# Kernel optimization log

Hardware: AMD Instinct MI355X
Metric: run time of the kernel (lower is better)

## Reference

```python
import jax, jax.numpy as jnp
import numpy as np

N = 100000   # num 'note' nodes
E = 1000000  # edges per relation
R = 3        # relation types (onset, consecutive, during)
IN = 128
OUT = 64
NEG_SLOPE = 0.2  # GATConv default leaky_relu slope


def setup_inputs() -> dict:
    key = jax.random.key(0)
    ks = jax.random.split(key, 13)
    x = jax.random.normal(ks[0], (N, IN), jnp.float32)
    ei0 = jax.random.randint(ks[1], (2, E), 0, N)
    ei1 = jax.random.randint(ks[2], (2, E), 0, N)
    ei2 = jax.random.randint(ks[3], (2, E), 0, N)
    s1 = 1.0 / np.sqrt(IN)
    s2 = 1.0 / np.sqrt(OUT)
    W1 = jax.random.normal(ks[4], (R, IN, OUT), jnp.float32) * s1
    a_src1 = jax.random.normal(ks[5], (R, OUT), jnp.float32) * s2
    a_dst1 = jax.random.normal(ks[6], (R, OUT), jnp.float32) * s2
    b1 = jnp.zeros((R, OUT), jnp.float32)
    W2 = jax.random.normal(ks[7], (R, OUT, OUT), jnp.float32) * s2
    a_src2 = jax.random.normal(ks[8], (R, OUT), jnp.float32) * s2
    a_dst2 = jax.random.normal(ks[9], (R, OUT), jnp.float32) * s2
    b2 = jnp.zeros((R, OUT), jnp.float32)
    return dict(x=x, ei0=ei0, ei1=ei1, ei2=ei2,
                W1=W1, a_src1=a_src1, a_dst1=a_dst1, b1=b1,
                W2=W2, a_src2=a_src2, a_dst2=a_dst2, b2=b2)


def _gat_relation(x, ei, W, a_src, a_dst, b):
    # single-head GATConv for one relation (aggr='sum' over edges)
    h = x @ W                              # [N, OUT]
    src, dst = ei[0], ei[1]
    al_src = h @ a_src                     # [N]
    al_dst = h @ a_dst                     # [N]
    e = jax.nn.leaky_relu(al_src[src] + al_dst[dst], NEG_SLOPE)  # [E]
    # segment softmax over incoming edges per destination node
    m = jax.ops.segment_max(e, dst, num_segments=N)              # [N]
    num = jnp.exp(e - m[dst])                                    # [E]
    den = jax.ops.segment_sum(num, dst, num_segments=N)          # [N]
    coef = num / den[dst]                                        # [E]
    msg = coef[:, None] * h[src]                                 # [E, OUT]
    return jax.ops.segment_sum(msg, dst, num_segments=N) + b     # [N, OUT]


def _hetero_layer(x, eis, W, a_src, a_dst, b):
    # to_hetero: per-relation GATConv, then mean across relations
    outs = [_gat_relation(x, eis[r], W[r], a_src[r], a_dst[r], b[r]) for r in range(R)]
    return jnp.mean(jnp.stack(outs, 0), 0)


def _l2norm(v):
    # F.normalize(v, dim=-1), eps=1e-12
    n = jnp.linalg.norm(v, axis=-1, keepdims=True)
    return v / jnp.maximum(n, 1e-12)


def reference(x, ei0, ei1, ei2, W1, a_src1, a_dst1, b1, W2, a_src2, a_dst2, b2):
    eis = [ei0, ei1, ei2]
    h = _hetero_layer(x, eis, W1, a_src1, a_dst1, b1)
    h = jax.nn.relu(_l2norm(h))  # dropout is identity in eval mode
    out = _hetero_layer(h, eis, W2, a_src2, a_dst2, b2)
    return out  # x_dict['note']
```

## Files before the change

### kernel.cpp

```cpp
#include <hip/hip_runtime.h>
#include <hip/hip_bf16.h>
#include <hip/hip_fp16.h>
#include <math.h>

constexpr int NN = 100000;
constexpr int EE = 1000000;
constexpr int RRR = 3;
constexpr int DIN = 128;
constexpr int DOUT = 64;
constexpr float SLOPE = 0.2f;
constexpr int NR = RRR * NN;
constexpr int BSEG = 256;
constexpr int NBUCK = (NR + BSEG - 1) / BSEG;
constexpr int BCAP = 4096;
constexpr int CHUNK_E = 4096;
constexpr int NCH_PER_R = (EE + CHUNK_E - 1) / CHUNK_E;
constexpr int NCH = RRR * NCH_PER_R;
constexpr int MT = NBUCK * NCH;
constexpr int SCAN_CHUNK = 1024;
constexpr int NSCB = (MT + SCAN_CHUNK - 1) / SCAN_CHUNK;
constexpr int GEMM_BLKS = (NN + 63) / 64;

using f16x8 = __attribute__((ext_vector_type(8))) _Float16;
using f32x4 = __attribute__((ext_vector_type(4))) float;

template<int CTRL>
__device__ __forceinline__ float dppf(float v) {
    return __int_as_float(__builtin_amdgcn_update_dpp(
        __float_as_int(v), __float_as_int(v), CTRL, 0xf, 0xf, false));
}
__device__ __forceinline__ float dpp_allred_add16(float v) {
    v += dppf<0xB1>(v);
    v += dppf<0x4E>(v);
    v += dppf<0x141>(v);
    v += dppf<0x140>(v);
    return v;
}

__global__ __launch_bounds__(256) void pack_W(
    const float* __restrict__ W1, const float* __restrict__ W2,
    const float* __restrict__ b1, const float* __restrict__ b2,
    __half* __restrict__ Wp1, __half* __restrict__ Wp2,
    float* __restrict__ bs1, float* __restrict__ bs2)
{
    int r = blockIdx.x;
    for (int i = threadIdx.x; i < 4 * 4 * 512; i += 256) {
        int j = i & 7, lane = (i >> 3) & 63, nt = (i >> 9) & 3, ks = i >> 11;
        int k = ks * 32 + (lane >> 4) * 8 + j, c = nt * 16 + (lane & 15);
        Wp1[((size_t)r * 16 + ks * 4 + nt) * 512 + lane * 8 + j] = __float2half(W1[(r * DIN + k) * 64 + c]);
    }
    for (int i = threadIdx.x; i < 2 * 4 * 512; i += 256) {
        int j = i & 7, lane = (i >> 3) & 63, nt = (i >> 9) & 3, ks = i >> 11;
        int k = ks * 32 + (lane >> 4) * 8 + j, c = nt * 16 + (lane & 15);
        Wp2[((size_t)r * 8 + ks * 4 + nt) * 512 + lane * 8 + j] = __float2half(W2[(r * DOUT + k) * 64 + c]);
    }
    if (r == 0) {
        for (int c = threadIdx.x; c < 64; c += 256) {
            bs1[c] = (b1[c] + b1[64 + c] + b1[128 + c]) * (1.f / 3.f);
            bs2[c] = (b2[c] + b2[64 + c] + b2[128 + c]) * (1.f / 3.f);
        }
    }
}

template<int K, typename AT>
__device__ __forceinline__ void gemm_body(
    int gbid,
    const AT* __restrict__ xin,
    const __half* __restrict__ Wp,
    const float* __restrict__ asrc, const float* __restrict__ adst,
    __half* __restrict__ h,
    float* __restrict__ als, float* __restrict__ ald)
{
    constexpr int KS = K / 32;
    __shared__ float outb[64 * 65];
    const int t = threadIdx.x;
    const int lane = t & 63;
    const int w = t >> 6;
    const int row0 = gbid * 64;

    const int kgrp = lane >> 4;
    const int l15 = lane & 15;
    int arow = row0 + w * 16 + l15; if (arow >= NN) arow = NN - 1;

    f16x8 a[KS];
    if constexpr (sizeof(AT) == 2) {
        const __half* ab = (const __half*)xin + (size_t)arow * K + kgrp * 8;
#pragma unroll
        for (int ks = 0; ks < KS; ++ks) a[ks] = *(const f16x8*)(ab + ks * 32);
    } else {
        const float* ab = (const float*)xin + (size_t)arow * K + kgrp * 8;
#pragma unroll
        for (int ks = 0; ks < KS; ++ks) {
            float4 lo = *(const float4*)(ab + ks * 32);
            float4 hi = *(const float4*)(ab + ks * 32 + 4);
            union { f16x8 v; __half2 p[4]; } u;
            u.p[0] = __floats2half2_rn(lo.x, lo.y);
            u.p[1] = __floats2half2_rn(lo.z, lo.w);
            u.p[2] = __floats2half2_rn(hi.x, hi.y);
            u.p[3] = __floats2half2_rn(hi.z, hi.w);
            a[ks] = u.v;
        }
    }

    const int nrows = (NN - row0 < 64) ? (NN - row0) : 64;

#pragma unroll
    for (int r = 0; r < RRR; ++r) {
        const __half* wbase = Wp + ((size_t)r * KS * 4) * 512 + lane * 8;
        f32x4 acc[4] = {};
#pragma unroll
        for (int ks = 0; ks < KS; ++ks) {
#pragma unroll
            for (int nt = 0; nt < 4; ++nt) {
                f16x8 b = *(const f16x8*)(wbase + (size_t)(ks * 4 + nt) * 512);
                acc[nt] = __builtin_amdgcn_mfma_f32_16x16x32_f16(a[ks], b, acc[nt], 0, 0, 0);
            }
        }

        {
            float ps[4] = {0.f, 0.f, 0.f, 0.f}, pd[4] = {0.f, 0.f, 0.f, 0.f};
#pragma unroll
            for (int nt = 0; nt < 4; ++nt) {
                int c = l15 + 16 * nt;
                float a_ = asrc[r * 64 + c], d_ = adst[r * 64 + c];
#pragma unroll
                for (int i = 0; i < 4; ++i) {
                    ps[i] = fmaf(acc[nt][i], a_, ps[i]);
                    pd[i] = fmaf(acc[nt][i], d_, pd[i]);
                }
            }
#pragma unroll
            for (int o = 8; o; o >>= 1) {
#pragma unroll
                for (int i = 0; i < 4; ++i) {
                    ps[i] += __shfl_xor(ps[i], o);
                    pd[i] += __shfl_xor(pd[i], o);
                }
            }
            if (l15 == 0) {
#pragma unroll
                for (int i = 0; i < 4; ++i) {
                    int row = row0 + w * 16 + kgrp * 4 + i;
                    if (row < NN) { als[r * NN + row] = ps[i]; ald[r * NN + row] = pd[i]; }
                }
            }
        }

#pragma unroll
        for (int nt = 0; nt < 4; ++nt)
#pragma unroll
            for (int i = 0; i < 4; ++i)
                outb[(w * 16 + kgrp * 4 + i) * 65 + l15 + 16 * nt] = acc[nt][i];
        __syncthreads();

        __half2* h2 = (__half2*)(h + ((size_t)r * NN + row0) * 64);
        for (int idx = t; idx < nrows * 32; idx += 256) {
            int row = idx >> 5, cc = idx & 31;
            h2[row * 32 + cc] = __floats2half2_rn(outb[row * 65 + cc * 2], outb[row * 65 + cc * 2 + 1]);
        }
        __syncthreads();
    }
}

__device__ __forceinline__ void hist_body(
    int hb,
    const int* __restrict__ ei0, const int* __restrict__ ei1, const int* __restrict__ ei2,
    unsigned* __restrict__ M)
{
    __shared__ unsigned hist[NBUCK];
    const int r = hb / NCH_PER_R, bx = hb % NCH_PER_R;
    const int* ei = (r == 0) ? ei0 : ((r == 1) ? ei1 : ei2);
    const int t = threadIdx.x;
    for (int i = t; i < NBUCK; i += 256) hist[i] = 0;
    __syncthreads();
    const int e0 = bx * CHUNK_E;
    const int e1 = (e0 + CHUNK_E < EE) ? e0 + CHUNK_E : EE;
    for (int e = e0 + t; e < e1; e += 256) {
        int idx = r * NN + ei[EE + e];
        atomicAdd(&hist[idx >> 8], 1u);
    }
    __syncthreads();
    const int c = r * NCH_PER_R + bx;
    for (int i = t; i < NBUCK; i += 256) M[(size_t)i * NCH + c] = hist[i];
}

__global__ __launch_bounds__(256) void fused_prep(
    const float* __restrict__ x, const __half* __restrict__ Wp1,
    const float* __restrict__ as1, const float* __restrict__ ad1,
    __half* __restrict__ h, float* __restrict__ als, float* __restrict__ ald,
    const int* __restrict__ ei0, const int* __restrict__ ei1, const int* __restrict__ ei2,
    unsigned* __restrict__ M)
{
    if ((int)blockIdx.x < GEMM_BLKS)
        gemm_body<DIN, float>(blockIdx.x, x, Wp1, as1, ad1, h, als, ald);
    else
        hist_body(blockIdx.x - GEMM_BLKS, ei0, ei1, ei2, M);
}

template<int K, typename AT>
__global__ __launch_bounds__(256) void gemm_mfma2(
    const AT* __restrict__ xin, const __half* __restrict__ Wp,
    const float* __restrict__ asrc, const float* __restrict__ adst,
    __half* __restrict__ h, float* __restrict__ als, float* __restrict__ ald)
{
    gemm_body<K, AT>(blockIdx.x, xin, Wp, asrc, adst, h, als, ald);
}

__global__ __launch_bounds__(256) void scan_block(unsigned* __restrict__ data, unsigned* __restrict__ bsum)
{
    __shared__ unsigned tsum[256];
    const int base = blockIdx.x * SCAN_CHUNK;
    const int t = threadIdx.x;
    const int i0 = base + t * 4;
    unsigned v[4];
#pragma unroll
    for (int k = 0; k < 4; ++k) v[k] = (i0 + k < MT) ? data[i0 + k] : 0u;
    unsigned run = 0;
#pragma unroll
    for (int k = 0; k < 4; ++k) { unsigned x = v[k]; v[k] = run; run += x; }
    tsum[t] = run;
    __syncthreads();
    unsigned val = run;
    for (int d = 1; d < 256; d <<= 1) {
        unsigned add = (t >= d) ? tsum[t - d] : 0u;
        __syncthreads();
        val += add;
        tsum[t] = val;
        __syncthreads();
    }
    unsigned texcl = val - run;
    if (t == 255) bsum[blockIdx.x] = val;
#pragma unroll
    for (int k = 0; k < 4; ++k)
        if (i0 + k < MT) data[i0 + k] = texcl + v[k];
}

__global__ __launch_bounds__(256) void scan_add(unsigned* __restrict__ data, const unsigned* __restrict__ bsum)
{
    __shared__ unsigned red[256];
    const int b = blockIdx.x, t = threadIdx.x;
    unsigned part = 0;
    for (int j = t; j < b; j += 256) part += bsum[j];
    red[t] = part;
    __syncthreads();
    for (int s = 128; s; s >>= 1) {
        if (t < s) red[t] += red[t + s];
        __syncthreads();
    }
    unsigned P = red[0];
    const int i0 = b * SCAN_CHUNK + t * 4;
#pragma unroll
    for (int k = 0; k < 4; ++k)
        if (i0 + k < MT) data[i0 + k] += P;
}

__global__ __launch_bounds__(256) void chunk_scatter(
    const int* __restrict__ ei0, const int* __restrict__ ei1, const int* __restrict__ ei2,
    const unsigned* __restrict__ Ms, unsigned* __restrict__ packed)
{
    __shared__ unsigned cur[NBUCK];
    const int r = blockIdx.y, bx = blockIdx.x;
    const int* ei = (r == 0) ? ei0 : ((r == 1) ? ei1 : ei2);
    const int t = threadIdx.x;
    const int c = r * NCH_PER_R + bx;
    for (int i = t; i < NBUCK; i += 256) cur[i] = Ms[(size_t)i * NCH + c];
    __syncthreads();
    const int e0 = bx * CHUNK_E;
    const int e1 = (e0 + CHUNK_E < EE) ? e0 + CHUNK_E : EE;
    for (int e = e0 + t; e < e1; e += 256) {
        int src = ei[e];
        int idx = r * NN + ei[EE + e];
        unsigned pos = atomicAdd(&cur[idx >> 8], 1u);
        packed[pos] = (unsigned)src | ((unsigned)(idx & 255) << 24);
    }
}

__global__ __launch_bounds__(256) void bucket_build(
    unsigned* __restrict__ packed,
    const unsigned* __restrict__ Ms,
    unsigned* __restrict__ off)
{
    __shared__ unsigned sp[BCAP];
    __shared__ unsigned ssrc[BCAP];
    __shared__ unsigned scnt[BSEG];
    __shared__ unsigned scur[BSEG];
    __shared__ unsigned tsum[BSEG];
    const int b = blockIdx.x;
    const int t = threadIdx.x;
    const unsigned base = Ms[(size_t)b * NCH];
    const unsigned next = (b + 1 < NBUCK) ? Ms[(size_t)(b + 1) * NCH] : (unsigned)((size_t)RRR * EE);
    int cnt = (int)(next - base);
    if (cnt > BCAP) cnt = BCAP;
    for (int i = t; i < cnt; i += 256) sp[i] = packed[base + i];
    scnt[t] = 0;
    __syncthreads();
    for (int i = t; i < cnt; i += 256) atomicAdd(&scnt[sp[i] >> 24], 1u);
    __syncthreads();
    unsigned v = scnt[t];
    tsum[t] = v;
    __syncthreads();
    unsigned val = v;
    for (int d = 1; d < 256; d <<= 1) {
        unsigned add = (t >= d) ? tsum[t - d] : 0u;
        __syncthreads();
        val += add;
        tsum[t] = val;
        __syncthreads();
    }
    unsigned excl = val - v;
    scur[t] = excl;
    const int segs = (NR - b * BSEG < BSEG) ? (NR - b * BSEG) : BSEG;
    if (t < segs) off[b * BSEG + t] = base + excl;
    __syncthreads();
    for (int i = t; i < cnt; i += 256) {
        unsigned p = sp[i];
        unsigned pos = atomicAdd(&scur[p >> 24], 1u);
        ssrc[pos] = p & 0x00FFFFFFu;
    }
    __syncthreads();
    for (int i = t; i < cnt; i += 256) packed[base + i] = ssrc[i];
}

template<bool L1>
__global__ __launch_bounds__(256) void aggregate10(
    const int* __restrict__ csr_src, const unsigned* __restrict__ off,
    const __half* __restrict__ h,
    const float* __restrict__ als, const float* __restrict__ ald,
    const float* __restrict__ bsum3,
    float* __restrict__ outp,
    __half* __restrict__ outH)
{
    __shared__ float sbuf[4][64];
    const int wid = threadIdx.x >> 6;
    const int lane = threadIdx.x & 63;
    const int nh = lane >> 5;
    const int l31 = lane & 31;
    const int sub = l31 >> 4;
    const int fc = l31 & 15;
    const int node = blockIdx.x * 8 + wid * 2 + nh;

    unsigned start[RRR]; int cnt[RRR]; float aldv[RRR];
    int maxcnt = 0;
#pragma unroll
    for (int r = 0; r < RRR; ++r) {
        int idx = r * NN + node;
        unsigned s = off[idx];
        unsigned e = (idx == NR - 1) ? (unsigned)((size_t)RRR * EE) : off[idx + 1];
        start[r] = s; cnt[r] = (int)(e - s); aldv[r] = ald[idx];
        if (cnt[r] > maxcnt) maxcnt = cnt[r];
    }

    float4 total = make_float4(0.f, 0.f, 0.f, 0.f);

    if (__all(maxcnt <= 32)) {
        int srcv[RRR]; float p[RRR], den[RRR];
#pragma unroll
        for (int r = 0; r < RRR; ++r) {
            bool act = l31 < cnt[r];
            int s_ = act ? csr_src[start[r] + l31] : 0;
            srcv[r] = s_;
            float sv = act ? (als[r * NN + s_] + aldv[r]) : -3.0e38f;
            float lr = (sv > 0.f) ? sv : SLOPE * sv;
            lr = fminf(lr, 60.f);
            p[r] = __expf(lr);
            den[r] = dpp_allred_add16(p[r]);
        }
#pragma unroll
        for (int r = 0; r < RRR; ++r) den[r] += __shfl_xor(den[r], 16);
#pragma unroll
        for (int r = 0; r < RRR; ++r) {
            float inv = (cnt[r] > 0) ? 1.f / den[r] : 0.f;
            p[r] *= inv;
        }

        float4 acc = make_float4(0.f, 0.f, 0.f, 0.f);
#pragma unroll
        for (int r = 0; r < RRR; ++r) {
            const __half* hr = h + (size_t)r * NN * DOUT;
            const int nq = (cnt[r] + 7) >> 3;
            for (int q = 0; q < nq; ++q) {
                const int base = q * 8;
                float pl[4]; int sl[4];
#pragma unroll
                for (int l = 0; l < 4; ++l) {
                    int e = base + l * 2 + sub;
                    pl[l] = __shfl(p[r], nh * 32 + e);
                    sl[l] = __shfl(srcv[r], nh * 32 + e);
                }
                uint2 rl[4];
#pragma unroll
                for (int l = 0; l < 4; ++l)
                    rl[l] = *(const uint2*)(hr + (size_t)sl[l] * DOUT + fc * 4);
#pragma unroll
                for (int l = 0; l < 4; ++l) {
                    float2 f01 = __half22float2(*(const __half2*)&rl[l].x);
                    float2 f23 = __half22float2(*(const __half2*)&rl[l].y);
                    acc.x = fmaf(pl[l], f01.x, acc.x);
                    acc.y = fmaf(pl[l], f01.y, acc.y);
                    acc.z = fmaf(pl[l], f23.x, acc.z);
                    acc.w = fmaf(pl[l], f23.y, acc.w);
                }
            }
        }
        acc.x += __shfl_xor(acc.x, 16); acc.y += __shfl_xor(acc.y, 16);
        acc.z += __shfl_xor(acc.z, 16); acc.w += __shfl_xor(acc.w, 16);
        total = acc;
    } else {
        for (int nn = 0; nn < 2; ++nn) {
            int node2 = blockIdx.x * 8 + wid * 2 + nn;
            float totalS = 0.f;
#pragma unroll
            for (int r = 0; r < RRR; ++r) {
                int idx = r * NN + node2;
                unsigned s2 = off[idx];
                unsigned e2 = (idx == NR - 1) ? (unsigned)((size_t)RRR * EE) : off[idx + 1];
                int c2 = (int)(e2 - s2);
                if (c2 <= 0) continue;
                float aldv2 = ald[idx];
                const __half* hr = h + (size_t)r * NN * DOUT;
                const float* alsr = als + (size_t)r * NN;
                float m = -3.4e38f, den = 0.f, accv = 0.f;
                for (int t0 = 0; t0 < c2; t0 += 64) {
                    int j = t0 + lane;
                    bool act = (j < c2);
                    int src = 0;
                    float lrv = -3.4e38f;
                    if (act) {
                        src = csr_src[s2 + j];
                        float sv = alsr[src] + aldv2;
                        lrv = (sv > 0.f) ? sv : SLOPE * sv;
                    }
                    float mt = lrv;
#pragma unroll
                    for (int o = 32; o; o >>= 1) mt = fmaxf(mt, __shfl_xor(mt, o));
                    float mnew = fmaxf(m, mt);
                    float scale = __expf(m - mnew);
                    den *= scale; accv *= scale; m = mnew;
                    float pp = act ? __expf(lrv - m) : 0.f;
                    float ps = pp;
#pragma unroll
                    for (int o = 32; o; o >>= 1) ps += __shfl_xor(ps, o);
                    den += ps;
                    int tcnt = c2 - t0; if (tcnt > 64) tcnt = 64;
                    for (int j2 = 0; j2 < tcnt; ++j2) {
                        int sj = __builtin_amdgcn_readlane(src, j2);
                        float pj = __int_as_float(__builtin_amdgcn_readlane(__float_as_int(pp), j2));
                        accv = fmaf(pj, __half2float(hr[(size_t)sj * DOUT + lane]), accv);
                    }
                }
                totalS += accv / den;
            }
            sbuf[wid][lane] = totalS;
            __builtin_amdgcn_s_waitcnt(0);
            if (nh == nn) total = *(const float4*)&sbuf[wid][fc * 4];
            __builtin_amdgcn_s_waitcnt(0);
        }
    }

    float4 bb = *(const float4*)(bsum3 + fc * 4);
    float4 v;
    v.x = fmaf(total.x, 1.f / 3.f, bb.x);
    v.y = fmaf(total.y, 1.f / 3.f, bb.y);
    v.z = fmaf(total.z, 1.f / 3.f, bb.z);
    v.w = fmaf(total.w, 1.f / 3.f, bb.w);
    if (L1) {
        float ss = v.x * v.x + v.y * v.y + v.z * v.z + v.w * v.w;
        ss = dpp_allred_add16(ss);
        float di = 1.f / fmaxf(sqrtf(ss), 1e-12f);
        v.x = fmaxf(v.x * di, 0.f);
        v.y = fmaxf(v.y * di, 0.f);
        v.z = fmaxf(v.z * di, 0.f);
        v.w = fmaxf(v.w * di, 0.f);
        if (sub == 0) {
            __half2* o2 = (__half2*)(outH + (size_t)node * DOUT + fc * 4);
            o2[0] = __floats2half2_rn(v.x, v.y);
            o2[1] = __floats2half2_rn(v.z, v.w);
        }
    } else {
        if (sub == 0) *(float4*)(outp + (size_t)node * DOUT + fc * 4) = v;
    }
}

extern "C" void kernel_launch(void* const* d_in, const int* in_sizes, int n_in,
                              void* d_out, int out_size, void* d_ws, size_t ws_size,
                              hipStream_t stream) {
    const float* x   = (const float*)d_in[0];
    const int* ei0   = (const int*)d_in[1];
    const int* ei1   = (const int*)d_in[2];
    const int* ei2   = (const int*)d_in[3];
    const float* W1  = (const float*)d_in[4];
    const float* as1 = (const float*)d_in[5];
    const float* ad1 = (const float*)d_in[6];
    const float* b1  = (const float*)d_in[7];
    const float* W2  = (const float*)d_in[8];
    const float* as2 = (const float*)d_in[9];
    const float* ad2 = (const float*)d_in[10];
    const float* b2  = (const float*)d_in[11];
    float* out = (float*)d_out;

    float* ws = (float*)d_ws;
    size_t off_u = 0;
    __half* h       = (__half*)(ws + off_u); off_u += (size_t)RRR * NN * DOUT / 2;
    float* als      = ws + off_u; off_u += (size_t)RRR * NN;
    float* ald      = ws + off_u; off_u += (size_t)RRR * NN;
    unsigned* packed= (unsigned*)(ws + off_u); off_u += (size_t)RRR * EE;
    unsigned* off   = (unsigned*)(ws + off_u); off_u += NR;
    __half* hmid_h  = (__half*)(ws + off_u); off_u += (size_t)NN * DOUT / 2;
    __half* Wp1     = (__half*)(ws + off_u); off_u += (3 * 16 * 512) / 2;
    __half* Wp2     = (__half*)(ws + off_u); off_u += (3 * 8 * 512) / 2;
    float* bs1      = ws + off_u; off_u += 64;
    float* bs2      = ws + off_u; off_u += 64;
    unsigned* M     = (unsigned*)(ws + off_u); off_u += MT;
    unsigned* bsum  = (unsigned*)(ws + off_u); off_u += NSCB + 8;

    dim3 blk(256);
    dim3 gC(NCH_PER_R, RRR);
    int gA = (NN + 7) / 8;

    pack_W<<<3, blk, 0, stream>>>(W1, W2, b1, b2, Wp1, Wp2, bs1, bs2);

    fused_prep<<<GEMM_BLKS + NCH, blk, 0, stream>>>(
        x, Wp1, as1, ad1, h, als, ald, ei0, ei1, ei2, M);

    scan_block<<<NSCB, blk, 0, stream>>>(M, bsum);
    scan_add<<<NSCB, blk, 0, stream>>>(M, bsum);
    chunk_scatter<<<gC, blk, 0, stream>>>(ei0, ei1, ei2, M, packed);
    bucket_build<<<NBUCK, blk, 0, stream>>>(packed, M, off);
    const int* csr_src = (const int*)packed;

    aggregate10<true><<<gA, blk, 0, stream>>>(csr_src, off, h, als, ald, bs1, out, hmid_h);

    gemm_mfma2<DOUT, __half><<<GEMM_BLKS, blk, 0, stream>>>(hmid_h, Wp2, as2, ad2, h, als, ald);
    aggregate10<false><<<gA, blk, 0, stream>>>(csr_src, off, h, als, ald, bs2, out, hmid_h);
}
```

Measured before the change: 256.8 us.

## Fuse CSR scan, scatter and bucket build into one cooperative kernel

Replaces four separate launches (block scan, scan add, chunk scatter, bucket build) with a single cooperative kernel that uses grid-wide syncs between phases, launched with NCH blocks. This removes per-kernel launch gaps and tail effects. In exchange, each grid.sync has its own cost, the scan and bucket phases now run with fewer blocks in grid-stride loops, and the 33KB shared allocation limits residency, which cooperative launch requires for all blocks.

```diff
diff --git a/kernel.cpp b/kernel.cpp
--- a/kernel.cpp
+++ b/kernel.cpp
@@ -1,7 +1,10 @@
 #include <hip/hip_runtime.h>
+#include <hip/hip_cooperative_groups.h>
 #include <hip/hip_bf16.h>
 #include <hip/hip_fp16.h>
 #include <math.h>
+
+namespace cg = cooperative_groups;
 
 constexpr int NN = 100000;
 constexpr int EE = 1000000;
@@ -206,119 +209,128 @@
     gemm_body<K, AT>(blockIdx.x, xin, Wp, asrc, adst, h, als, ald);
 }
 
-__global__ __launch_bounds__(256) void scan_block(unsigned* __restrict__ data, unsigned* __restrict__ bsum)
-{
-    __shared__ unsigned tsum[256];
-    const int base = blockIdx.x * SCAN_CHUNK;
+__global__ __launch_bounds__(256) void csr_finish(
+    const int* __restrict__ ei0, const int* __restrict__ ei1, const int* __restrict__ ei2,
+    unsigned* __restrict__ M, unsigned* __restrict__ bsum,
+    unsigned* __restrict__ packed, unsigned* __restrict__ off)
+{
+    __shared__ unsigned smem[2 * BCAP + 3 * BSEG];
+    cg::grid_group grid = cg::this_grid();
     const int t = threadIdx.x;
-    const int i0 = base + t * 4;
-    unsigned v[4];
-#pragma unroll
-    for (int k = 0; k < 4; ++k) v[k] = (i0 + k < MT) ? data[i0 + k] : 0u;
-    unsigned run = 0;
-#pragma unroll
-    for (int k = 0; k < 4; ++k) { unsigned x = v[k]; v[k] = run; run += x; }
-    tsum[t] = run;
-    __syncthreads();
-    unsigned val = run;
-    for (int d = 1; d < 256; d <<= 1) {
-        unsigned add = (t >= d) ? tsum[t - d] : 0u;
+    const int nb = gridDim.x;
+
+    {
+        unsigned* tsum = smem;
+        for (int b = blockIdx.x; b < NSCB; b += nb) {
+            __syncthreads();
+            const int i0 = b * SCAN_CHUNK + t * 4;
+            unsigned v[4];
+#pragma unroll
+            for (int k = 0; k < 4; ++k) v[k] = (i0 + k < MT) ? M[i0 + k] : 0u;
+            unsigned run = 0;
+#pragma unroll
+            for (int k = 0; k < 4; ++k) { unsigned x = v[k]; v[k] = run; run += x; }
+            tsum[t] = run;
+            __syncthreads();
+            unsigned val = run;
+            for (int d = 1; d < 256; d <<= 1) {
+                unsigned add = (t >= d) ? tsum[t - d] : 0u;
+                __syncthreads();
+                val += add;
+                tsum[t] = val;
+                __syncthreads();
+            }
+            unsigned texcl = val - run;
+            if (t == 255) bsum[b] = val;
+#pragma unroll
+            for (int k = 0; k < 4; ++k)
+                if (i0 + k < MT) M[i0 + k] = texcl + v[k];
+        }
+    }
+    grid.sync();
+
+    {
+        unsigned* red = smem;
+        for (int b = blockIdx.x; b < NSCB; b += nb) {
+            __syncthreads();
+            unsigned part = 0;
+            for (int j = t; j < b; j += 256) part += bsum[j];
+            red[t] = part;
+            __syncthreads();
+            for (int s = 128; s; s >>= 1) {
+                if (t < s) red[t] += red[t + s];
+                __syncthreads();
+            }
+            unsigned P = red[0];
+            const int i0 = b * SCAN_CHUNK + t * 4;
+#pragma unroll
+            for (int k = 0; k < 4; ++k)
+                if (i0 + k < MT) M[i0 + k] += P;
+        }
+    }
+    grid.sync();
+
+    {
+        unsigned* cur = smem;
+        const int hb = blockIdx.x;
+        const int r = hb / NCH_PER_R, bx = hb % NCH_PER_R;
+        const int* ei = (r == 0) ? ei0 : ((r == 1) ? ei1 : ei2);
         __syncthreads();
-        val += add;
-        tsum[t] = val;
+        for (int i = t; i < NBUCK; i += 256) cur[i] = M[(size_t)i * NCH + hb];
         __syncthreads();
-    }
-    unsigned texcl = val - run;
-    if (t == 255) bsum[blockIdx.x] = val;
-#pragma unroll
-    for (int k = 0; k < 4; ++k)
-        if (i0 + k < MT) data[i0 + k] = texcl + v[k];
-}
-
-__global__ __launch_bounds__(256) void scan_add(unsigned* __restrict__ data, const unsigned* __restrict__ bsum)
-{
-    __shared__ unsigned red[256];
-    const int b = blockIdx.x, t = threadIdx.x;
-    unsigned part = 0;
-    for (int j = t; j < b; j += 256) part += bsum[j];
-    red[t] = part;
-    __syncthreads();
-    for (int s = 128; s; s >>= 1) {
-        if (t < s) red[t] += red[t + s];
-        __syncthreads();
-    }
-    unsigned P = red[0];
-    const int i0 = b * SCAN_CHUNK + t * 4;
-#pragma unroll
-    for (int k = 0; k < 4; ++k)
-        if (i0 + k < MT) data[i0 + k] += P;
-}
-
-__global__ __launch_bounds__(256) void chunk_scatter(
-    const int* __restrict__ ei0, const int* __restrict__ ei1, const int* __restrict__ ei2,
-    const unsigned* __restrict__ Ms, unsigned* __restrict__ packed)
-{
-    __shared__ unsigned cur[NBUCK];
-    const int r = blockIdx.y, bx = blockIdx.x;
-    const int* ei = (r == 0) ? ei0 : ((r == 1) ? ei1 : ei2);
-    const int t = threadIdx.x;
-    const int c = r * NCH_PER_R + bx;
-    for (int i = t; i < NBUCK; i += 256) cur[i] = Ms[(size_t)i * NCH + c];
-    __syncthreads();
-    const int e0 = bx * CHUNK_E;
-    const int e1 = (e0 + CHUNK_E < EE) ? e0 + CHUNK_E : EE;
-    for (int e = e0 + t; e < e1; e += 256) {
-        int src = ei[e];
-        int idx = r * NN + ei[EE + e];
-        unsigned pos = atomicAdd(&cur[idx >> 8], 1u);
-        packed[pos] = (unsigned)src | ((unsigned)(idx & 255) << 24);
-    }
-}
-
-__global__ __launch_bounds__(256) void bucket_build(
-    unsigned* __restrict__ packed,
-    const unsigned* __restrict__ Ms,
-    unsigned* __restrict__ off)
-{
-    __shared__ unsigned sp[BCAP];
-    __shared__ unsigned ssrc[BCAP];
-    __shared__ unsigned scnt[BSEG];
-    __shared__ unsigned scur[BSEG];
-    __shared__ unsigned tsum[BSEG];
-    const int b = blockIdx.x;
-    const int t = threadIdx.x;
-    const unsigned base = Ms[(size_t)b * NCH];
-    const unsigned next = (b + 1 < NBUCK) ? Ms[(size_t)(b + 1) * NCH] : (unsigned)((size_t)RRR * EE);
-    int cnt = (int)(next - base);
-    if (cnt > BCAP) cnt = BCAP;
-    for (int i = t; i < cnt; i += 256) sp[i] = packed[base + i];
-    scnt[t] = 0;
-    __syncthreads();
-    for (int i = t; i < cnt; i += 256) atomicAdd(&scnt[sp[i] >> 24], 1u);
-    __syncthreads();
-    unsigned v = scnt[t];
-    tsum[t] = v;
-    __syncthreads();
-    unsigned val = v;
-    for (int d = 1; d < 256; d <<= 1) {
-        unsigned add = (t >= d) ? tsum[t - d] : 0u;
-        __syncthreads();
-        val += add;
-        tsum[t] = val;
-        __syncthreads();
-    }
-    unsigned excl = val - v;
-    scur[t] = excl;
-    const int segs = (NR - b * BSEG < BSEG) ? (NR - b * BSEG) : BSEG;
-    if (t < segs) off[b * BSEG + t] = base + excl;
-    __syncthreads();
-    for (int i = t; i < cnt; i += 256) {
-        unsigned p = sp[i];
-        unsigned pos = atomicAdd(&scur[p >> 24], 1u);
-        ssrc[pos] = p & 0x00FFFFFFu;
-    }
-    __syncthreads();
-    for (int i = t; i < cnt; i += 256) packed[base + i] = ssrc[i];
+        const int e0 = bx * CHUNK_E;
+        const int e1 = (e0 + CHUNK_E < EE) ? e0 + CHUNK_E : EE;
+        for (int e = e0 + t; e < e1; e += 256) {
+            int src = ei[e];
+            int idx = r * NN + ei[EE + e];
+            unsigned pos = atomicAdd(&cur[idx >> 8], 1u);
+            packed[pos] = (unsigned)src | ((unsigned)(idx & 255) << 24);
+        }
+    }
+    grid.sync();
+
+    {
+        unsigned* sp   = smem;
+        unsigned* ssrc = smem + BCAP;
+        unsigned* scnt = smem + 2 * BCAP;
+        unsigned* scur = smem + 2 * BCAP + BSEG;
+        unsigned* ts2  = smem + 2 * BCAP + 2 * BSEG;
+        for (int b = blockIdx.x; b < NBUCK; b += nb) {
+            __syncthreads();
+            const unsigned base = M[(size_t)b * NCH];
+            const unsigned next = (b + 1 < NBUCK) ? M[(size_t)(b + 1) * NCH] : (unsigned)((size_t)RRR * EE);
+            int cnt = (int)(next - base);
+            if (cnt > BCAP) cnt = BCAP;
+            for (int i = t; i < cnt; i += 256) sp[i] = packed[base + i];
+            scnt[t] = 0;
+            __syncthreads();
+            for (int i = t; i < cnt; i += 256) atomicAdd(&scnt[sp[i] >> 24], 1u);
+            __syncthreads();
+            unsigned v = scnt[t];
+            ts2[t] = v;
+            __syncthreads();
+            unsigned val = v;
+            for (int d = 1; d < 256; d <<= 1) {
+                unsigned add = (t >= d) ? ts2[t - d] : 0u;
+                __syncthreads();
+                val += add;
+                ts2[t] = val;
+                __syncthreads();
+            }
+            unsigned excl = val - v;
+            scur[t] = excl;
+            const int segs = (NR - b * BSEG < BSEG) ? (NR - b * BSEG) : BSEG;
+            if (t < segs) off[b * BSEG + t] = base + excl;
+            __syncthreads();
+            for (int i = t; i < cnt; i += 256) {
+                unsigned p = sp[i];
+                unsigned pos = atomicAdd(&scur[p >> 24], 1u);
+                ssrc[pos] = p & 0x00FFFFFFu;
+            }
+            __syncthreads();
+            for (int i = t; i < cnt; i += 256) packed[base + i] = ssrc[i];
+        }
+    }
 }
 
 template<bool L1>
@@ -514,7 +526,6 @@
     unsigned* bsum  = (unsigned*)(ws + off_u); off_u += NSCB + 8;
 
     dim3 blk(256);
-    dim3 gC(NCH_PER_R, RRR);
     int gA = (NN + 7) / 8;
 
     pack_W<<<3, blk, 0, stream>>>(W1, W2, b1, b2, Wp1, Wp2, bs1, bs2);
@@ -522,10 +533,11 @@
     fused_prep<<<GEMM_BLKS + NCH, blk, 0, stream>>>(
         x, Wp1, as1, ad1, h, als, ald, ei0, ei1, ei2, M);
 
-    scan_block<<<NSCB, blk, 0, stream>>>(M, bsum);
-    scan_add<<<NSCB, blk, 0, stream>>>(M, bsum);
-    chunk_scatter<<<gC, blk, 0, stream>>>(ei0, ei1, ei2, M, packed);
-    bucket_build<<<NBUCK, blk, 0, stream>>>(packed, M, off);
+    {
+        void* args[] = { (void*)&ei0, (void*)&ei1, (void*)&ei2,
+                         (void*)&M, (void*)&bsum, (void*)&packed, (void*)&off };
+        hipLaunchCooperativeKernel((const void*)csr_finish, dim3(NCH), blk, args, 0, stream);
+    }
     const int* csr_src = (const int*)packed;
 
     aggregate10<true><<<gA, blk, 0, stream>>>(csr_src, off, h, als, ald, bs1, out, hmid_h);
```

After: 555.0 us. 2.16x slower.
